# Kernel tuning notes

Measured on AMD Instinct MI355X. Metric: run time of the kernel, lower is better.

## Reference

```python
import jax, jax.numpy as jnp
import numpy as np

H_DIM = 128
EMB = 16
MODES = 6
TRAJ = MODES * 2  # 12
PRED_LEN = 30
B = 65536
NEG_SLOPE = 0.01  # F.leaky_relu default


def setup_inputs() -> dict:
    key = jax.random.key(0)
    ks = jax.random.split(key, 16)
    s = lambda k, shape, fan_in: jax.random.uniform(k, shape, jnp.float32, -1.0, 1.0) / np.sqrt(fan_in)
    return {
        "last_obs": jax.random.normal(ks[0], (B, 2), jnp.float32),
        "last_obs_rel": jax.random.normal(ks[1], (B, 2), jnp.float32),
        "h0": jax.random.normal(ks[2], (1, B, H_DIM), jnp.float32),
        "c0": jax.random.normal(ks[3], (1, B, H_DIM), jnp.float32),
        # nn.LSTM(EMB, H_DIM, 1): weight_ih (4H, EMB), weight_hh (4H, H), biases (4H,)
        "W_ih": s(ks[4], (4 * H_DIM, EMB), H_DIM),
        "W_hh": s(ks[5], (4 * H_DIM, H_DIM), H_DIM),
        "b_ih": s(ks[6], (4 * H_DIM,), H_DIM),
        "b_hh": s(ks[7], (4 * H_DIM,), H_DIM),
        # spatial_embedding: Linear(TRAJ, EMB)
        "W_emb": s(ks[8], (EMB, TRAJ), TRAJ),
        "b_emb": s(ks[9], (EMB,), TRAJ),
        # hidden2pos: Linear(H_DIM, TRAJ)
        "W_pos": s(ks[10], (TRAJ, H_DIM), H_DIM),
        "b_pos": s(ks[11], (TRAJ,), H_DIM),
        # confidences: Linear(H_DIM, MODES)
        "W_conf": s(ks[12], (MODES, H_DIM), H_DIM),
        "b_conf": s(ks[13], (MODES,), H_DIM),
    }


def _lstm_cell(x, h, c, W_ih, W_hh, b):
    # x: (B, EMB), h/c: (B, H). PyTorch gate order: i, f, g, o
    gates = x @ W_ih.T + h @ W_hh.T + b  # (B, 4H)
    i, f, g, o = jnp.split(gates, 4, axis=-1)
    c_new = jax.nn.sigmoid(f) * c + jax.nn.sigmoid(i) * jnp.tanh(g)
    h_new = jax.nn.sigmoid(o) * jnp.tanh(c_new)
    return h_new, c_new


def reference(last_obs, last_obs_rel, h0, c0, W_ih, W_hh, b_ih, b_hh,
              W_emb, b_emb, W_pos, b_pos, W_conf, b_conf):
    b_gate = b_ih + b_hh
    batch = last_obs_rel.shape[0]
    # repeat_interleave last_obs_rel over modes -> (B, 12)
    rel0 = jnp.repeat(last_obs_rel[:, None, :], MODES, axis=1).reshape(batch, TRAJ)
    dec_in = jax.nn.leaky_relu(rel0 @ W_emb.T + b_emb, NEG_SLOPE)  # (B, EMB); eval mode => no dropout

    def step(carry, _):
        h, c, x = carry
        h, c = _lstm_cell(x, h, c, W_ih, W_hh, b_gate)
        rel_pos = h @ W_pos.T + b_pos                                # (B, TRAJ)
        x_next = jax.nn.leaky_relu(rel_pos @ W_emb.T + b_emb, NEG_SLOPE)
        return (h, c, x_next), rel_pos

    (_, _, _), rels = jax.lax.scan(step, (h0[0], c0[0], dec_in), None, length=PRED_LEN)
    # rels: (PRED_LEN, B, TRAJ) -> (B, MODES, PRED_LEN, 2)
    pred = rels.reshape(PRED_LEN, batch, MODES, 2).transpose(1, 2, 0, 3)
    # conf uses the ORIGINAL (un-updated) state_tuple_h, as in the source
    conf = jax.nn.softmax(h0[0] @ W_conf.T + b_conf, axis=1)         # (B, MODES)
    return pred, conf
```

## Files before the change

kernel.cpp:

```cpp
#include <hip/hip_runtime.h>

typedef _Float16 f16;
typedef f16 f16x2 __attribute__((ext_vector_type(2)));
typedef f16 f16x4 __attribute__((ext_vector_type(4)));
typedef f16 f16x8 __attribute__((ext_vector_type(8)));
typedef float f32x4 __attribute__((ext_vector_type(4)));
typedef __fp16 fp16x2_raw __attribute__((ext_vector_type(2)));

#define MT 64
#define NSTEP 30
#define LOG2E 1.4426950408889634f

__device__ __forceinline__ float rcp_f(float x) { return __builtin_amdgcn_rcpf(x); }
__device__ __forceinline__ float exp2_f(float x) {
#if __has_builtin(__builtin_amdgcn_exp2f)
    return __builtin_amdgcn_exp2f(x);
#else
    return __builtin_exp2f(x);
#endif
}
__device__ __forceinline__ f16x2 pk2(float a, float b) {
    fp16x2_raw t = __builtin_amdgcn_cvt_pkrtz(a, b);
    return __builtin_bit_cast(f16x2, t);
}
__device__ __forceinline__ f16x4 pk4(float a, float b, float c, float d) {
    f16x2 lo = pk2(a, b), hi = pk2(c, d);
    f16x4 r; r[0] = lo[0]; r[1] = lo[1]; r[2] = hi[0]; r[3] = hi[1];
    return r;
}

__global__ __launch_bounds__(512) void mdlstm_kernel(
    const float* __restrict__ lor,
    const float* __restrict__ h0,
    const float* __restrict__ c0,
    const float* __restrict__ W_ih,
    const float* __restrict__ W_hh,
    const float* __restrict__ b_ih, const float* __restrict__ b_hh,
    const float* __restrict__ W_emb,
    const float* __restrict__ b_emb,
    const float* __restrict__ W_pos,
    const float* __restrict__ b_pos,
    const float* __restrict__ W_conf,
    const float* __restrict__ b_conf,
    float* __restrict__ out, int batch)
{
    __shared__ f16 h_lds[2 * MT * 128];
    __shared__ f16 x_lds[MT * 16];
    __shared__ f16 rel_lds[MT * 16];
    __shared__ f16 wpos_lds[4 * 64 * 8];

    char* hb   = (char*)h_lds;
    char* xb   = (char*)x_lds;
    char* relb = (char*)rel_lds;
    char* wpb  = (char*)wpos_lds;

    const int tid = threadIdx.x;
    const int wv  = tid >> 6;
    const int ln  = tid & 63;
    const int g   = ln >> 4;
    const int q   = ln & 15;
    const int b0  = blockIdx.x * MT;
    if (b0 >= batch) return;

    const float gsc[4] = {-LOG2E, -LOG2E, 2.f * LOG2E, -LOG2E};

    f16x8 whh[4][4];
    #pragma unroll
    for (int g4 = 0; g4 < 4; ++g4) {
        const int col = g4 * 128 + wv * 16 + q;
        #pragma unroll
        for (int kf = 0; kf < 4; ++kf) {
            const float* p = W_hh + col * 128 + kf * 32 + g * 8;
            f16x8 v;
            #pragma unroll
            for (int j = 0; j < 8; ++j) v[j] = (f16)(p[j] * gsc[g4]);
            whh[g4][kf] = v;
        }
    }
    f16x8 wih[4];
    #pragma unroll
    for (int g4 = 0; g4 < 4; ++g4) {
        const int col = g4 * 128 + wv * 16 + q;
        f16x8 v = {};
        if (g < 2) {
            const float* p = W_ih + col * 16 + g * 8;
            #pragma unroll
            for (int j = 0; j < 8; ++j) v[j] = (f16)(p[j] * gsc[g4]);
        } else if (g == 2) {
            v[0] = (f16)((b_ih[col] + b_hh[col]) * gsc[g4]);
        }
        wih[g4] = v;
    }
    f16x8 wemb = {};
    #pragma unroll
    for (int j = 0; j < 8; ++j) {
        const int k = g * 8 + j;
        if (k < 12) wemb[j] = (f16)W_emb[q * 12 + k];
    }
    f32x4 bembv, bposv;
    #pragma unroll
    for (int r = 0; r < 4; ++r) {
        bembv[r] = b_emb[4 * g + r];
        bposv[r] = (4 * g + r < 12) ? b_pos[4 * g + r] : 0.f;
    }

    if (wv == 0) {
        #pragma unroll
        for (int kf = 0; kf < 4; ++kf) {
            f16x8 v = {};
            if (q < 12) {
                const float* p = W_pos + q * 128 + kf * 32 + g * 8;
                #pragma unroll
                for (int j = 0; j < 8; ++j) v[j] = (f16)p[j];
            }
            *(f16x8*)(wpb + kf * 1024 + ln * 16) = v;
        }
    }

    f32x4 c_st[4];
    #pragma unroll
    for (int mt = 0; mt < 4; ++mt)
        c_st[mt] = *(const f32x4*)(c0 + (size_t)(b0 + 16 * mt + q) * 128 + 16 * wv + 4 * g);

    const int swz = (q & 7) << 5;
    int rdbase[4];
    #pragma unroll
    for (int kf = 0; kf < 4; ++kf) rdbase[kf] = q * 256 + ((kf * 64 + g * 16) ^ swz);
    const int wrb = q * 256 + ((wv * 32 + g * 8) ^ swz);
    const int xrd = q * 32 + g * 16;
    const int xwr = q * 32 + g * 8;

    float* outp = out + (size_t)(b0 + 16 * wv + q) * 360 + 2 * g * 60;

    {
        const int row = tid >> 3, seg = tid & 7;
        const float* p = h0 + (size_t)(b0 + row) * 128 + seg * 16;
        const int rswz = (row & 7) << 5;
        #pragma unroll
        for (int hh = 0; hh < 2; ++hh) {
            f16x8 v;
            #pragma unroll
            for (int j = 0; j < 8; ++j) v[j] = (f16)p[hh * 8 + j];
            const int off = row * 256 + (((seg * 4 + 2 * hh) * 8) ^ rswz);
            *(f16x8*)(hb + off) = v;
        }
    }

    if (wv < 4) {
        const float2 xy = *(const float2*)(lor + (size_t)(b0 + 16 * wv + q) * 2);
        f16x8 rf = {};
        if (g < 2) {
            #pragma unroll
            for (int j = 0; j < 8; ++j) {
                const int k = g * 8 + j;
                if (k < 12) rf[j] = (f16)((k & 1) ? xy.y : xy.x);
            }
        }
        f32x4 xacc = bembv;
        xacc = __builtin_amdgcn_mfma_f32_16x16x32_f16(wemb, rf, xacc, 0, 0, 0);
        f16x4 xp = pk4(fmaxf(xacc[0], .01f * xacc[0]), fmaxf(xacc[1], .01f * xacc[1]),
                       fmaxf(xacc[2], .01f * xacc[2]), fmaxf(xacc[3], .01f * xacc[3]));
        *(f16x4*)(xb + wv * 512 + xwr) = xp;
    }

    {
        const int e  = tid >> 3;
        const int p8 = tid & 7;
        const float* hp = h0 + (size_t)(b0 + e) * 128 + p8 * 16;
        float pc[6];
        #pragma unroll
        for (int md = 0; md < 6; ++md) {
            const float* wc = W_conf + md * 128 + p8 * 16;
            float s = 0.f;
            #pragma unroll
            for (int i = 0; i < 16; ++i) s += hp[i] * wc[i];
            pc[md] = s;
        }
        #pragma unroll
        for (int md = 0; md < 6; ++md) {
            pc[md] += __shfl_down(pc[md], 4, 8);
            pc[md] += __shfl_down(pc[md], 2, 8);
            pc[md] += __shfl_down(pc[md], 1, 8);
        }
        if (p8 == 0) {
            float mx = -1e30f;
            #pragma unroll
            for (int md = 0; md < 6; ++md) { pc[md] += b_conf[md]; mx = fmaxf(mx, pc[md]); }
            float s = 0.f;
            #pragma unroll
            for (int md = 0; md < 6; ++md) { pc[md] = __expf(pc[md] - mx); s += pc[md]; }
            const float rs = rcp_f(s);
            float* cp = out + (size_t)batch * 360 + (size_t)(b0 + e) * 6;
            #pragma unroll
            for (int md = 0; md < 6; ++md) cp[md] = pc[md] * rs;
        }
    }

    __syncthreads();

#define STEP(BR, BW, T_) do {                                                   \
    _Pragma("unroll")                                                           \
    for (int mt = 0; mt < 4; ++mt) {                                            \
        f32x4 a0 = {0,0,0,0}, a1 = {0,0,0,0}, a2 = {0,0,0,0}, a3 = {0,0,0,0};   \
        _Pragma("unroll")                                                       \
        for (int kf = 0; kf < 4; ++kf) {                                        \
            f16x8 hf = *(const f16x8*)(hb + (BR) + mt * 4096 + rdbase[kf]);     \
            a0 = __builtin_amdgcn_mfma_f32_16x16x32_f16(whh[0][kf], hf, a0, 0, 0, 0); \
            a1 = __builtin_amdgcn_mfma_f32_16x16x32_f16(whh[1][kf], hf, a1, 0, 0, 0); \
            a2 = __builtin_amdgcn_mfma_f32_16x16x32_f16(whh[2][kf], hf, a2, 0, 0, 0); \
            a3 = __builtin_amdgcn_mfma_f32_16x16x32_f16(whh[3][kf], hf, a3, 0, 0, 0); \
        }                                                                       \
        {                                                                       \
            f16x8 xf = {};                                                      \
            if (g < 2)       xf = *(const f16x8*)(xb + mt * 512 + xrd);         \
            else if (g == 2) xf[0] = (f16)1.f;                                  \
            a0 = __builtin_amdgcn_mfma_f32_16x16x32_f16(wih[0], xf, a0, 0, 0, 0); \
            a1 = __builtin_amdgcn_mfma_f32_16x16x32_f16(wih[1], xf, a1, 0, 0, 0); \
            a2 = __builtin_amdgcn_mfma_f32_16x16x32_f16(wih[2], xf, a2, 0, 0, 0); \
            a3 = __builtin_amdgcn_mfma_f32_16x16x32_f16(wih[3], xf, a3, 0, 0, 0); \
        }                                                                       \
        f32x4 hv;                                                               \
        _Pragma("unroll")                                                       \
        for (int r = 0; r < 4; ++r) {                                           \
            const float ei = exp2_f(a0[r]);                                     \
            const float ef = exp2_f(a1[r]);                                     \
            const float eg = exp2_f(a2[r]);                                     \
            const float eo = exp2_f(a3[r]);                                     \
            const float sf  = rcp_f(1.f + ef);                                  \
            const float itg = (eg - 1.f) * rcp_f((1.f + ei) * (1.f + eg));      \
            const float cv  = sf * c_st[mt][r] + itg;                           \
            c_st[mt][r] = cv;                                                   \
            const float ec = exp2_f(fminf(cv, 30.f) * (2.f * LOG2E));           \
            hv[r] = (ec - 1.f) * rcp_f((1.f + eo) * (1.f + ec));                \
        }                                                                       \
        *(f16x4*)(hb + (BW) + mt * 4096 + wrb) = pk4(hv[0], hv[1], hv[2], hv[3]); \
    }                                                                           \
    __syncthreads();                                            \
    if (wv < 4) {                                                               \
        f32x4 racc = bposv;                                                     \
        _Pragma("unroll")                                                       \
        for (int kf = 0; kf < 4; ++kf) {                                        \
            f16x8 wp = *(const f16x8*)(wpb + kf * 1024 + ln * 16);              \
            f16x8 hf = *(const f16x8*)(hb + (BW) + wv * 4096 + rdbase[kf]);     \
            racc = __builtin_amdgcn_mfma_f32_16x16x32_f16(wp, hf, racc, 0, 0, 0); \
        }                                                                       \
        if (g < 3) {                                                            \
            float2 s0 = {racc[0], racc[1]};                                     \
            float2 s1 = {racc[2], racc[3]};                                     \
            float* pp = outp + 2 * (T_);                                        \
            *(float2*)pp = s0;                                                  \
            *(float2*)(pp + 60) = s1;                                           \
        }                                                                       \
        *(f16x4*)(relb + wv * 512 + xwr) = pk4(racc[0], racc[1], racc[2], racc[3]); \
        __threadfence_block();                                                  \
        f16x8 rf = {};                                                          \
        if (g < 2) rf = *(const f16x8*)(relb + wv * 512 + xrd);                 \
        f32x4 xacc = bembv;                                                     \
        xacc = __builtin_amdgcn_mfma_f32_16x16x32_f16(wemb, rf, xacc, 0, 0, 0); \
        f16x4 xp = pk4(fmaxf(xacc[0], .01f * xacc[0]), fmaxf(xacc[1], .01f * xacc[1]), \
                       fmaxf(xacc[2], .01f * xacc[2]), fmaxf(xacc[3], .01f * xacc[3])); \
        *(f16x4*)(xb + wv * 512 + xwr) = xp;                                    \
    }                                                                           \
    __syncthreads();                                          \
} while (0)

    #pragma unroll 1
    for (int tt = 0; tt < NSTEP; tt += 2) {
        STEP(0, 16384, tt);
        STEP(16384, 0, tt + 1);
    }
#undef STEP
}

extern "C" void kernel_launch(void* const* d_in, const int* in_sizes, int n_in,
                              void* d_out, int out_size, void* d_ws, size_t ws_size,
                              hipStream_t stream) {
    const float* last_obs_rel = (const float*)d_in[1];
    const float* h0     = (const float*)d_in[2];
    const float* c0     = (const float*)d_in[3];
    const float* W_ih   = (const float*)d_in[4];
    const float* W_hh   = (const float*)d_in[5];
    const float* b_ih   = (const float*)d_in[6];
    const float* b_hh   = (const float*)d_in[7];
    const float* W_emb  = (const float*)d_in[8];
    const float* b_emb  = (const float*)d_in[9];
    const float* W_pos  = (const float*)d_in[10];
    const float* b_pos  = (const float*)d_in[11];
    const float* W_conf = (const float*)d_in[12];
    const float* b_conf = (const float*)d_in[13];
    float* out = (float*)d_out;

    const int batch = in_sizes[1] / 2;
    const int grid  = (batch + MT - 1) / MT;
    mdlstm_kernel<<<grid, 512, 0, stream>>>(last_obs_rel, h0, c0, W_ih, W_hh,
                                            b_ih, b_hh, W_emb, b_emb, W_pos,
                                            b_pos, W_conf, b_conf, out, batch);
}
```

Measured before the change: 461.1 us.

## Fold hidden2pos into embedding weights to drop a sync per LSTM step

Precomputes the composed matrix W_emb·W_pos and bias W_emb·b_pos + b_emb, so each step computes the next input embedding directly from the previous h inside the gate MFMA loop. The result is moved between lanes with shuffles instead of through LDS. The rel_pos output projection is delayed by one step so it reads the previous h buffer, which removes one __syncthreads and the LDS round-trip per step. It also fuses the sigmoid reciprocals into a single rcp and adds an occupancy hint to launch_bounds. In exchange there is one extra MFMA per k-fragment, and rounding changes slightly because the composed weights are stored in fp16.

After: 1.765 ms. +282.9%, slower.

```diff
diff --git a/kernel.cpp b/kernel.cpp
--- a/kernel.cpp
+++ b/kernel.cpp
@@ -5,6 +5,7 @@
 typedef f16 f16x4 __attribute__((ext_vector_type(4)));
 typedef f16 f16x8 __attribute__((ext_vector_type(8)));
 typedef float f32x4 __attribute__((ext_vector_type(4)));
+typedef int i32x4 __attribute__((ext_vector_type(4)));
 typedef __fp16 fp16x2_raw __attribute__((ext_vector_type(2)));
 
 #define MT 64
@@ -19,17 +20,17 @@
     return __builtin_exp2f(x);
 #endif
 }
-__device__ __forceinline__ f16x2 pk2(float a, float b) {
+__device__ __forceinline__ int pk2i(float a, float b) {
     fp16x2_raw t = __builtin_amdgcn_cvt_pkrtz(a, b);
-    return __builtin_bit_cast(f16x2, t);
+    return __builtin_bit_cast(int, t);
 }
 __device__ __forceinline__ f16x4 pk4(float a, float b, float c, float d) {
-    f16x2 lo = pk2(a, b), hi = pk2(c, d);
-    f16x4 r; r[0] = lo[0]; r[1] = lo[1]; r[2] = hi[0]; r[3] = hi[1];
-    return r;
-}
-
-__global__ __launch_bounds__(512) void mdlstm_kernel(
+    int lo = pk2i(a, b), hi = pk2i(c, d);
+    int2 t = {lo, hi};
+    return __builtin_bit_cast(f16x4, t);
+}
+
+__global__ __launch_bounds__(512, 4) void mdlstm_kernel(
     const float* __restrict__ lor,
     const float* __restrict__ h0,
     const float* __restrict__ c0,
@@ -45,14 +46,12 @@
     float* __restrict__ out, int batch)
 {
     __shared__ f16 h_lds[2 * MT * 128];
-    __shared__ f16 x_lds[MT * 16];
-    __shared__ f16 rel_lds[MT * 16];
     __shared__ f16 wpos_lds[4 * 64 * 8];
-
-    char* hb   = (char*)h_lds;
-    char* xb   = (char*)x_lds;
-    char* relb = (char*)rel_lds;
-    char* wpb  = (char*)wpos_lds;
+    __shared__ f16 weu_lds[4 * 64 * 8];
+
+    char* hb  = (char*)h_lds;
+    char* wpb = (char*)wpos_lds;
+    char* wub = (char*)weu_lds;
 
     const int tid = threadIdx.x;
     const int wv  = tid >> 6;
@@ -91,17 +90,19 @@
         }
         wih[g4] = v;
     }
-    f16x8 wemb = {};
-    #pragma unroll
-    for (int j = 0; j < 8; ++j) {
-        const int k = g * 8 + j;
-        if (k < 12) wemb[j] = (f16)W_emb[q * 12 + k];
-    }
-    f32x4 bembv, bposv;
+    f32x4 bposv;
+    #pragma unroll
+    for (int r = 0; r < 4; ++r)
+        bposv[r] = (4 * g + r < 12) ? b_pos[4 * g + r] : 0.f;
+
+    f32x4 buv;
     #pragma unroll
     for (int r = 0; r < 4; ++r) {
-        bembv[r] = b_emb[4 * g + r];
-        bposv[r] = (4 * g + r < 12) ? b_pos[4 * g + r] : 0.f;
+        const int e = 4 * g + r;
+        float s = b_emb[e];
+        #pragma unroll
+        for (int p = 0; p < 12; ++p) s += W_emb[e * 12 + p] * b_pos[p];
+        buv[r] = s;
     }
 
     if (wv == 0) {
@@ -115,6 +116,22 @@
             }
             *(f16x8*)(wpb + kf * 1024 + ln * 16) = v;
         }
+        float we_q[12];
+        #pragma unroll
+        for (int p = 0; p < 12; ++p) we_q[p] = W_emb[q * 12 + p];
+        #pragma unroll
+        for (int kf = 0; kf < 4; ++kf) {
+            f16x8 v;
+            #pragma unroll
+            for (int j = 0; j < 8; ++j) {
+                const int k = kf * 32 + g * 8 + j;
+                float s = 0.f;
+                #pragma unroll
+                for (int p = 0; p < 12; ++p) s += we_q[p] * W_pos[p * 128 + k];
+                v[j] = (f16)s;
+            }
+            *(f16x8*)(wub + kf * 1024 + ln * 16) = v;
+        }
     }
 
     f32x4 c_st[4];
@@ -127,8 +144,8 @@
     #pragma unroll
     for (int kf = 0; kf < 4; ++kf) rdbase[kf] = q * 256 + ((kf * 64 + g * 16) ^ swz);
     const int wrb = q * 256 + ((wv * 32 + g * 8) ^ swz);
-    const int xrd = q * 32 + g * 16;
-    const int xwr = q * 32 + g * 8;
+    const int src0 = ((g & 1) << 5) | q;
+    const int src1 = src0 + 16;
 
     float* outp = out + (size_t)(b0 + 16 * wv + q) * 360 + 2 * g * 60;
 
@@ -137,30 +154,42 @@
         const float* p = h0 + (size_t)(b0 + row) * 128 + seg * 16;
         const int rswz = (row & 7) << 5;
         #pragma unroll
-        for (int hh = 0; hh < 2; ++hh) {
+        for (int hh2 = 0; hh2 < 2; ++hh2) {
             f16x8 v;
             #pragma unroll
-            for (int j = 0; j < 8; ++j) v[j] = (f16)p[hh * 8 + j];
-            const int off = row * 256 + (((seg * 4 + 2 * hh) * 8) ^ rswz);
+            for (int j = 0; j < 8; ++j) v[j] = (f16)p[hh2 * 8 + j];
+            const int off = row * 256 + (((seg * 4 + 2 * hh2) * 8) ^ rswz);
             *(f16x8*)(hb + off) = v;
         }
     }
 
-    if (wv < 4) {
-        const float2 xy = *(const float2*)(lor + (size_t)(b0 + 16 * wv + q) * 2);
-        f16x8 rf = {};
-        if (g < 2) {
-            #pragma unroll
-            for (int j = 0; j < 8; ++j) {
-                const int k = g * 8 + j;
-                if (k < 12) rf[j] = (f16)((k & 1) ? xy.y : xy.x);
+    int d0s[4], d1s[4];
+    {
+        f16x8 wemb = {};
+        #pragma unroll
+        for (int j = 0; j < 8; ++j) {
+            const int k = g * 8 + j;
+            if (k < 12) wemb[j] = (f16)W_emb[q * 12 + k];
+        }
+        f32x4 bet;
+        #pragma unroll
+        for (int r = 0; r < 4; ++r) bet[r] = b_emb[4 * g + r];
+        #pragma unroll
+        for (int mt = 0; mt < 4; ++mt) {
+            const float2 xy = *(const float2*)(lor + (size_t)(b0 + mt * 16 + q) * 2);
+            f16x8 rf = {};
+            if (g < 2) {
+                #pragma unroll
+                for (int j = 0; j < 8; ++j) {
+                    const int k = g * 8 + j;
+                    if (k < 12) rf[j] = (f16)((k & 1) ? xy.y : xy.x);
+                }
             }
-        }
-        f32x4 xacc = bembv;
-        xacc = __builtin_amdgcn_mfma_f32_16x16x32_f16(wemb, rf, xacc, 0, 0, 0);
-        f16x4 xp = pk4(fmaxf(xacc[0], .01f * xacc[0]), fmaxf(xacc[1], .01f * xacc[1]),
-                       fmaxf(xacc[2], .01f * xacc[2]), fmaxf(xacc[3], .01f * xacc[3]));
-        *(f16x4*)(xb + wv * 512 + xwr) = xp;
+            f32x4 u0 = bet;
+            u0 = __builtin_amdgcn_mfma_f32_16x16x32_f16(wemb, rf, u0, 0, 0, 0);
+            d0s[mt] = pk2i(fmaxf(u0[0], .01f * u0[0]), fmaxf(u0[1], .01f * u0[1]));
+            d1s[mt] = pk2i(fmaxf(u0[2], .01f * u0[2]), fmaxf(u0[3], .01f * u0[3]));
+        }
     }
 
     {
@@ -198,10 +227,11 @@
 
     __syncthreads();
 
-#define STEP(BR, BW, T_) do {                                                   \
+#define STEP(BR, BW, T_, FIRST) do {                                            \
     _Pragma("unroll")                                                           \
     for (int mt = 0; mt < 4; ++mt) {                                            \
         f32x4 a0 = {0,0,0,0}, a1 = {0,0,0,0}, a2 = {0,0,0,0}, a3 = {0,0,0,0};   \
+        f32x4 uacc = buv;                                                       \
         _Pragma("unroll")                                                       \
         for (int kf = 0; kf < 4; ++kf) {                                        \
             f16x8 hf = *(const f16x8*)(hb + (BR) + mt * 4096 + rdbase[kf]);     \
@@ -209,16 +239,30 @@
             a1 = __builtin_amdgcn_mfma_f32_16x16x32_f16(whh[1][kf], hf, a1, 0, 0, 0); \
             a2 = __builtin_amdgcn_mfma_f32_16x16x32_f16(whh[2][kf], hf, a2, 0, 0, 0); \
             a3 = __builtin_amdgcn_mfma_f32_16x16x32_f16(whh[3][kf], hf, a3, 0, 0, 0); \
-        }                                                                       \
-        {                                                                       \
-            f16x8 xf = {};                                                      \
-            if (g < 2)       xf = *(const f16x8*)(xb + mt * 512 + xrd);         \
-            else if (g == 2) xf[0] = (f16)1.f;                                  \
-            a0 = __builtin_amdgcn_mfma_f32_16x16x32_f16(wih[0], xf, a0, 0, 0, 0); \
-            a1 = __builtin_amdgcn_mfma_f32_16x16x32_f16(wih[1], xf, a1, 0, 0, 0); \
-            a2 = __builtin_amdgcn_mfma_f32_16x16x32_f16(wih[2], xf, a2, 0, 0, 0); \
-            a3 = __builtin_amdgcn_mfma_f32_16x16x32_f16(wih[3], xf, a3, 0, 0, 0); \
-        }                                                                       \
+            if (!(FIRST)) {                                                     \
+                f16x8 wu = *(const f16x8*)(wub + kf * 1024 + ln * 16);          \
+                uacc = __builtin_amdgcn_mfma_f32_16x16x32_f16(wu, hf, uacc, 0, 0, 0); \
+            }                                                                   \
+        }                                                                       \
+        int d0i, d1i;                                                           \
+        if (FIRST) { d0i = d0s[mt]; d1i = d1s[mt]; }                            \
+        else {                                                                  \
+            d0i = pk2i(fmaxf(uacc[0], .01f * uacc[0]), fmaxf(uacc[1], .01f * uacc[1])); \
+            d1i = pk2i(fmaxf(uacc[2], .01f * uacc[2]), fmaxf(uacc[3], .01f * uacc[3])); \
+        }                                                                       \
+        const int w0 = __shfl(d0i, src0, 64);                                   \
+        const int w1 = __shfl(d1i, src0, 64);                                   \
+        const int w2 = __shfl(d0i, src1, 64);                                   \
+        const int w3 = __shfl(d1i, src1, 64);                                   \
+        i32x4 xw;                                                               \
+        if (g < 2)      { xw[0] = w0; xw[1] = w1; xw[2] = w2; xw[3] = w3; }     \
+        else if (g == 2){ xw[0] = 0x3C00; xw[1] = 0; xw[2] = 0; xw[3] = 0; }    \
+        else            { xw[0] = 0; xw[1] = 0; xw[2] = 0; xw[3] = 0; }         \
+        const f16x8 xf = __builtin_bit_cast(f16x8, xw);                         \
+        a0 = __builtin_amdgcn_mfma_f32_16x16x32_f16(wih[0], xf, a0, 0, 0, 0);   \
+        a1 = __builtin_amdgcn_mfma_f32_16x16x32_f16(wih[1], xf, a1, 0, 0, 0);   \
+        a2 = __builtin_amdgcn_mfma_f32_16x16x32_f16(wih[2], xf, a2, 0, 0, 0);   \
+        a3 = __builtin_amdgcn_mfma_f32_16x16x32_f16(wih[3], xf, a3, 0, 0, 0);   \
         f32x4 hv;                                                               \
         _Pragma("unroll")                                                       \
         for (int r = 0; r < 4; ++r) {                                           \
@@ -226,48 +270,61 @@
             const float ef = exp2_f(a1[r]);                                     \
             const float eg = exp2_f(a2[r]);                                     \
             const float eo = exp2_f(a3[r]);                                     \
-            const float sf  = rcp_f(1.f + ef);                                  \
-            const float itg = (eg - 1.f) * rcp_f((1.f + ei) * (1.f + eg));      \
-            const float cv  = sf * c_st[mt][r] + itg;                           \
+            const float pi = 1.f + ei, pf = 1.f + ef, pg = 1.f + eg;            \
+            const float t1 = pi * pg;                                           \
+            const float R1 = rcp_f(t1 * pf);                                    \
+            const float sf = t1 * R1;                                           \
+            const float itg = (eg - 1.f) * (pf * R1);                           \
+            const float cv = sf * c_st[mt][r] + itg;                            \
             c_st[mt][r] = cv;                                                   \
             const float ec = exp2_f(fminf(cv, 30.f) * (2.f * LOG2E));           \
-            hv[r] = (ec - 1.f) * rcp_f((1.f + eo) * (1.f + ec));                \
+            const float R2 = rcp_f((1.f + eo) * (1.f + ec));                    \
+            hv[r] = (ec - 1.f) * R2;                                            \
         }                                                                       \
         *(f16x4*)(hb + (BW) + mt * 4096 + wrb) = pk4(hv[0], hv[1], hv[2], hv[3]); \
     }                                                                           \
-    __syncthreads();                                            \
-    if (wv < 4) {                                                               \
+    if (!(FIRST) && wv < 4) {     \
         f32x4 racc = bposv;                                                     \
         _Pragma("unroll")                                                       \
         for (int kf = 0; kf < 4; ++kf) {                                        \
             f16x8 wp = *(const f16x8*)(wpb + kf * 1024 + ln * 16);              \
-            f16x8 hf = *(const f16x8*)(hb + (BW) + wv * 4096 + rdbase[kf]);     \
+            f16x8 hf = *(const f16x8*)(hb + (BR) + wv * 4096 + rdbase[kf]);     \
             racc = __builtin_amdgcn_mfma_f32_16x16x32_f16(wp, hf, racc, 0, 0, 0); \
         }                                                                       \
         if (g < 3) {                                                            \
             float2 s0 = {racc[0], racc[1]};                                     \
             float2 s1 = {racc[2], racc[3]};                                     \
-            float* pp = outp + 2 * (T_);                                        \
+            float* pp = outp + 2 * ((T_) - 1);                                  \
             *(float2*)pp = s0;                                                  \
             *(float2*)(pp + 60) = s1;                                           \
         }                                                                       \
-        *(f16x4*)(relb + wv * 512 + xwr) = pk4(racc[0], racc[1], racc[2], racc[3]); \
-        __threadfence_block();                                                  \
-        f16x8 rf = {};                                                          \
-        if (g < 2) rf = *(const f16x8*)(relb + wv * 512 + xrd);                 \
-        f32x4 xacc = bembv;                                                     \
-        xacc = __builtin_amdgcn_mfma_f32_16x16x32_f16(wemb, rf, xacc, 0, 0, 0); \
-        f16x4 xp = pk4(fmaxf(xacc[0], .01f * xacc[0]), fmaxf(xacc[1], .01f * xacc[1]), \
-                       fmaxf(xacc[2], .01f * xacc[2]), fmaxf(xacc[3], .01f * xacc[3])); \
-        *(f16x4*)(xb + wv * 512 + xwr) = xp;                                    \
     }                                                                           \
-    __syncthreads();                                          \
+    __syncthreads();                                                            \
 } while (0)
 
+    STEP(0, 16384, 0, true);
     #pragma unroll 1
-    for (int tt = 0; tt < NSTEP; tt += 2) {
-        STEP(0, 16384, tt);
-        STEP(16384, 0, tt + 1);
+    for (int tt = 1; tt < NSTEP - 1; tt += 2) {
+        STEP(16384, 0, tt, false);
+        STEP(0, 16384, tt + 1, false);
+    }
+    STEP(16384, 0, NSTEP - 1, false);
+
+    if (wv < 4) {
+        f32x4 racc = bposv;
+        #pragma unroll
+        for (int kf = 0; kf < 4; ++kf) {
+            f16x8 wp = *(const f16x8*)(wpb + kf * 1024 + ln * 16);
+            f16x8 hf = *(const f16x8*)(hb + wv * 4096 + rdbase[kf]);
+            racc = __builtin_amdgcn_mfma_f32_16x16x32_f16(wp, hf, racc, 0, 0, 0);
+        }
+        if (g < 3) {
+            float2 s0 = {racc[0], racc[1]};
+            float2 s1 = {racc[2], racc[3]};
+            float* pp = outp + 2 * (NSTEP - 1);
+            *(float2*)pp = s0;
+            *(float2*)(pp + 60) = s1;
+        }
     }
 #undef STEP
 }
```
